# Optimization experiments

Hardware: AMD Instinct MI355X
Metric: run time of the kernel (lower is better)

Reference implementation:

```python
import jax, jax.numpy as jnp
import numpy as np

N_NODES = 50000
N_EDGES = 400000
N_GRAPHS = 64
DIMS = [3, 24, 48, 192]


def gcn_conv(x, src, dst, deg_inv_sqrt, W, b, num_nodes):
    # PyG GCNConv: x' = D^{-1/2} (A + I) D^{-1/2} (X W) + b
    h = x @ W  # [N, out]
    norm = deg_inv_sqrt[src] * deg_inv_sqrt[dst]  # [E2]
    msg = h[src] * norm[:, None]  # gather + scale, [E2, out]
    out = jax.ops.segment_sum(msg, dst, num_segments=num_nodes)
    return out + b


def setup_inputs() -> dict:
    key = jax.random.key(0)
    ks = jax.random.split(key, 10)
    node_features = jax.random.normal(ks[0], (N_NODES, DIMS[0]), dtype=jnp.float32)
    edge_indices = jax.random.randint(ks[1], (2, N_EDGES), 0, N_NODES, dtype=jnp.int64)
    batch_indices = jnp.sort(jax.random.randint(ks[2], (N_NODES,), 0, N_GRAPHS, dtype=jnp.int64))
    params = {}
    for i in range(3):
        fan_in, fan_out = DIMS[i], DIMS[i + 1]
        scale = 1.0 / np.sqrt(fan_in)
        params[f"W{i+1}"] = jax.random.uniform(ks[3 + 2 * i], (fan_in, fan_out), minval=-scale, maxval=scale, dtype=jnp.float32)
        params[f"b{i+1}"] = jnp.zeros((fan_out,), dtype=jnp.float32)
    return dict(node_features=node_features, edge_indices=edge_indices,
                batch_indices=batch_indices, **params)


def reference(node_features, edge_indices, batch_indices, W1, b1, W2, b2, W3, b3):
    num_nodes = node_features.shape[0]
    # add self-loops once, shared across the three convs
    loops = jnp.arange(num_nodes, dtype=edge_indices.dtype)
    src = jnp.concatenate([edge_indices[0], loops])
    dst = jnp.concatenate([edge_indices[1], loops])
    deg = jax.ops.segment_sum(jnp.ones_like(dst, dtype=node_features.dtype), dst,
                              num_segments=num_nodes)
    deg_inv_sqrt = jnp.where(deg > 0, jax.lax.rsqrt(jnp.maximum(deg, 1e-12)), 0.0)

    x = gcn_conv(node_features, src, dst, deg_inv_sqrt, W1, b1, num_nodes)
    x = gcn_conv(x, src, dst, deg_inv_sqrt, W2, b2, num_nodes)
    x = gcn_conv(x, src, dst, deg_inv_sqrt, W3, b3, num_nodes)

    # mean aggregation over nodes per graph
    sums = jax.ops.segment_sum(x, batch_indices, num_segments=N_GRAPHS)
    counts = jax.ops.segment_sum(jnp.ones((num_nodes,), dtype=x.dtype), batch_indices,
                                 num_segments=N_GRAPHS)
    return sums / jnp.maximum(counts, 1.0)[:, None]
```

## Files before the change

kernel.cpp:

```cpp
#include <hip/hip_runtime.h>

#define NN 50000
#define NE 400000
#define NG 64
#define NBK 196
#define CAP 2560
#define SB 98
#define EPB 4096

typedef unsigned int uint32;
typedef unsigned short uint16;


static __device__ __forceinline__ float wsum(float v) {
#pragma unroll
  for (int o = 32; o > 0; o >>= 1) v += __shfl_xor(v, o, 64);
  return v;
}

__global__ void __launch_bounds__(256) k_init(
    const float* __restrict__ x, const float* __restrict__ W1,
    const float* __restrict__ b1, const float* __restrict__ W2,
    const float* __restrict__ b2, const float* __restrict__ W3,
    float* __restrict__ W123, float* __restrict__ bW23, float* __restrict__ bW3,
    uint32* __restrict__ rsv, float* __restrict__ pooled, float* __restrict__ A) {
  int t = threadIdx.x, b = blockIdx.x;
  if (b == NBK) {
    __shared__ float w12[144];
    __shared__ float t48[48];
    if (t < 144) {
      int i = t / 48, k = t % 48;
      float s = 0.f;
      for (int j = 0; j < 24; ++j) s += W1[i * 24 + j] * W2[j * 48 + k];
      w12[t] = s;
    }
    if (t < 48) {
      float s = 0.f;
      for (int j = 0; j < 24; ++j) s += b1[j] * W2[j * 48 + t];
      t48[t] = s;
    }
    __syncthreads();
    if (t < 192) {
      float a0 = 0, a1 = 0, a2 = 0, ab = 0, ab3 = 0;
      for (int k = 0; k < 48; ++k) {
        float w3 = W3[k * 192 + t];
        a0 += w12[k] * w3;
        a1 += w12[48 + k] * w3;
        a2 += w12[96 + k] * w3;
        ab += t48[k] * w3;
        ab3 += b2[k] * w3;
      }
      W123[t] = a0;
      W123[192 + t] = a1;
      W123[384 + t] = a2;
      bW23[t] = ab;
      bW3[t] = ab3;
    }
    return;
  }
  if (b == 0) {
    rsv[t] = 0u;
    pooled[t] = 0.f;
    pooled[256 + t] = 0.f;
  }
  int n = b * 256 + t;
  if (n < NN) {
    float4 v;
    v.x = x[3 * n + 0];
    v.y = x[3 * n + 1];
    v.z = x[3 * n + 2];
    v.w = 1.0f;
    reinterpret_cast<float4*>(A)[n] = v;
  }
}

__global__ void __launch_bounds__(256) k_bscat(const int* __restrict__ src,
                                               const int* __restrict__ dst,
                                               uint32* __restrict__ rsv,
                                               uint32* __restrict__ ebuf) {
  __shared__ uint32 cnt[256];
  __shared__ uint32 base[256];
  int t = threadIdx.x;
  cnt[t] = 0u;
  __syncthreads();
  uint32 pk[16];
  uint32 bk[16];
  int e0 = blockIdx.x * EPB + t;
#pragma unroll
  for (int k = 0; k < 16; ++k) {
    int e = e0 + k * 256;
    uint32 b = 0xFFFFFFFFu, p = 0u;
    if (e < NE) {
      uint32 s = (uint32)src[e], d = (uint32)dst[e];
      b = d >> 8;
      p = s | ((d & 255u) << 16);
      atomicAdd(&cnt[b], 1u);
    }
    pk[k] = p;
    bk[k] = b;
  }
  __syncthreads();
  {
    uint32 c = cnt[t];
    base[t] = c ? (t * CAP + atomicAdd(&rsv[t], c)) : 0u;
    cnt[t] = 0u;
  }
  __syncthreads();
#pragma unroll
  for (int k = 0; k < 16; ++k) {
    if (bk[k] != 0xFFFFFFFFu) {
      uint32 slot = base[bk[k]] + atomicAdd(&cnt[bk[k]], 1u);
      ebuf[slot] = pk[k];
    }
  }
}

__global__ void __launch_bounds__(256) k_csr(const uint32* __restrict__ rsv,
                                             const uint32* __restrict__ ebuf,
                                             uint16* __restrict__ csr,
                                             uint2* __restrict__ offse,
                                             float2* __restrict__ drr,
                                             float* __restrict__ A) {
  __shared__ uint32 cnt[256];
  __shared__ uint32 scn[256];
  int b = blockIdx.x, t = threadIdx.x;
  uint32 lo = (uint32)b * CAP;
  uint32 hi = lo + rsv[b];
  cnt[t] = 0u;
  __syncthreads();
  for (uint32 i = lo + t; i < hi; i += 256) atomicAdd(&cnt[ebuf[i] >> 16], 1u);
  __syncthreads();
  uint32 c = cnt[t];
  scn[t] = c;
  __syncthreads();
  for (int o = 1; o < 256; o <<= 1) {
    uint32 u = (t >= o) ? scn[t - o] : 0u;
    __syncthreads();
    scn[t] += u;
    __syncthreads();
  }
  uint32 excl = scn[t] - c;
  cnt[t] = excl;
  int n = b * 256 + t;
  if (n < NN) {
    uint2 oe;
    oe.x = lo + excl;
    oe.y = lo + excl + c;
    offse[n] = oe;
    float deg = (float)(c + 1u);
    float ds = rsqrtf(deg);
    float2 dr;
    dr.x = 1.0f / deg;
    dr.y = sqrtf(deg);
    drr[n] = dr;
    float4 v4 = reinterpret_cast<const float4*>(A)[n];
    v4.x *= ds; v4.y *= ds; v4.z *= ds; v4.w *= ds;
    reinterpret_cast<float4*>(A)[n] = v4;
  }
  __syncthreads();
  for (uint32 i = lo + t; i < hi; i += 256) {
    uint32 p = ebuf[i];
    uint32 slot = atomicAdd(&cnt[p >> 16], 1u);
    csr[lo + slot] = (uint16)p;
  }
}

__global__ void k_gather(const uint2* __restrict__ offse,
                         const uint16* __restrict__ csr,
                         const float2* __restrict__ drr,
                         const float* __restrict__ zin, float* __restrict__ zout) {
  int tid = blockIdx.x * blockDim.x + threadIdx.x;
  int n = tid >> 2, ln = tid & 3;
  if (n >= NN) return;
  uint2 oe = offse[n];
  float4 acc = make_float4(0.f, 0.f, 0.f, 0.f);
  for (uint32 i = oe.x + ln; i < oe.y; i += 4) {
    uint32 s = csr[i];
    float4 v = reinterpret_cast<const float4*>(zin)[s];
    acc.x += v.x; acc.y += v.y; acc.z += v.z; acc.w += v.w;
  }
#pragma unroll
  for (int o = 1; o < 4; o <<= 1) {
    acc.x += __shfl_xor(acc.x, o, 64);
    acc.y += __shfl_xor(acc.y, o, 64);
    acc.z += __shfl_xor(acc.z, o, 64);
    acc.w += __shfl_xor(acc.w, o, 64);
  }
  if (ln == 0) {
    float4 zs = reinterpret_cast<const float4*>(zin)[n];
    float w = drr[n].x;
    float4 o4;
    o4.x = (acc.x + zs.x) * w;
    o4.y = (acc.y + zs.y) * w;
    o4.z = (acc.z + zs.z) * w;
    o4.w = (acc.w + zs.w) * w;
    reinterpret_cast<float4*>(zout)[n] = o4;
  }
}

__global__ void k_gather3_pool(const uint2* __restrict__ offse,
                               const uint16* __restrict__ csr,
                               const float2* __restrict__ drr,
                               const int* __restrict__ batch,
                               const float* __restrict__ B,
                               const float* __restrict__ C2,
                               float* __restrict__ pooled) {
  int tid = blockIdx.x * blockDim.x + threadIdx.x;
  int n = tid >> 2, ln = tid & 3;
  if (n >= NN) return;
  uint2 oe = offse[n];
  float ax = 0.f, ay = 0.f, az = 0.f;
  for (uint32 i = oe.x + ln; i < oe.y; i += 4) {
    uint32 s = csr[i];
    float4 v = reinterpret_cast<const float4*>(C2)[s];
    ax += v.x; ay += v.y; az += v.z;
  }
#pragma unroll
  for (int o = 1; o < 4; o <<= 1) {
    ax += __shfl_xor(ax, o, 64);
    ay += __shfl_xor(ay, o, 64);
    az += __shfl_xor(az, o, 64);
  }
  int g = batch[n];
  float vx = 0, vy = 0, vz = 0, v1 = 0, v2 = 0, cc = 0;
  if (ln == 0) {
    float4 zs = reinterpret_cast<const float4*>(C2)[n];
    float2 dr = drr[n];
    float rr = dr.y;
    float wr = dr.x * rr;
    vx = (ax + zs.x) * wr;
    vy = (ay + zs.y) * wr;
    vz = (az + zs.z) * wr;
    v1 = zs.w * rr;
    v2 = B[4 * n + 3] * rr;
    cc = 1.0f;
  }
  int g0 = __shfl(g, 0, 64);
  bool uni = __all(g == g0);
  if (uni) {
    float sx = wsum(vx), sy = wsum(vy), sz = wsum(vz);
    float s1 = wsum(v1), s2 = wsum(v2), sc = wsum(cc);
    if ((threadIdx.x & 63) == 0) {
      float* p = pooled + 8 * g0;
      atomicAdd(p + 0, sx); atomicAdd(p + 1, sy); atomicAdd(p + 2, sz);
      atomicAdd(p + 3, s1); atomicAdd(p + 4, s2); atomicAdd(p + 5, sc);
    }
  } else if (ln == 0) {
    float* p = pooled + 8 * g;
    atomicAdd(p + 0, vx); atomicAdd(p + 1, vy); atomicAdd(p + 2, vz);
    atomicAdd(p + 3, v1); atomicAdd(p + 4, v2); atomicAdd(p + 5, cc);
  }
}

__global__ void k_final(const float* __restrict__ pooled, const float* __restrict__ W123,
                        const float* __restrict__ bW23, const float* __restrict__ bW3,
                        const float* __restrict__ b3, float* __restrict__ out) {
  int g = blockIdx.x;
  int l = threadIdx.x;
  const float* p = pooled + 8 * g;
  float ic = 1.0f / fmaxf(p[5], 1.0f);
  float sx = p[0] * ic, sy = p[1] * ic, sz = p[2] * ic;
  float v1 = p[3] * ic, v2 = p[4] * ic;
  out[g * 192 + l] = sx * W123[l] + sy * W123[192 + l] + sz * W123[384 + l] +
                     v1 * bW23[l] + v2 * bW3[l] + b3[l];
}

extern "C" void kernel_launch(void* const* d_in, const int* in_sizes, int n_in,
                              void* d_out, int out_size, void* d_ws, size_t ws_size,
                              hipStream_t stream) {
  const float* x = (const float*)d_in[0];
  const int* edges = (const int*)d_in[1];
  const int* batch = (const int*)d_in[2];
  const float* W1 = (const float*)d_in[3];
  const float* b1 = (const float*)d_in[4];
  const float* W2 = (const float*)d_in[5];
  const float* b2 = (const float*)d_in[6];
  const float* W3 = (const float*)d_in[7];
  const float* b3 = (const float*)d_in[8];
  float* out = (float*)d_out;

  const int* src = edges;
  const int* dst = edges + NE;

  float* ws = (float*)d_ws;
  uint32* rsv = (uint32*)ws;
  uint2* offse = (uint2*)(ws + 256);
  float2* drr = (float2*)(ws + 100256);
  float* A = ws + 200256;
  float* B = ws + 400256;
  float* C2 = ws + 600256;
  uint32* ebuf = (uint32*)(ws + 800256);
  uint16* csr = (uint16*)(ws + 1302016);
  float* pooled = ws + 1552896;
  float* W123 = ws + 1553408;
  float* bW23 = ws + 1553984;
  float* bW3 = ws + 1554176;

  dim3 b256(256);
  dim3 bg((NN * 4 + 255) / 256);

  k_init<<<NBK + 1, b256, 0, stream>>>(x, W1, b1, W2, b2, W3, W123, bW23, bW3,
                                       rsv, pooled, A);
  k_bscat<<<SB, b256, 0, stream>>>(src, dst, rsv, ebuf);
  k_csr<<<NBK, b256, 0, stream>>>(rsv, ebuf, csr, offse, drr, A);

  k_gather<<<bg, b256, 0, stream>>>(offse, csr, drr, A, B);
  k_gather<<<bg, b256, 0, stream>>>(offse, csr, drr, B, C2);
  k_gather3_pool<<<bg, b256, 0, stream>>>(offse, csr, drr, batch, B, C2, pooled);

  k_final<<<NG, 192, 0, stream>>>(pooled, W123, bW23, bW3, b3, out);
}
```

Baseline: 61.33 us.

## Fuse edge bucketing into init kernel and final projection into last gather

Edge bucket-scatter now runs inside the init kernel. Each of 49 edge blocks writes into private per-(block,bucket) slots with fixed capacity, which removes the global reservation atomics. The CSR kernel reads these per-block segments using the stored counts. The final per-graph projection is folded into the last gather kernel through a last-block-done counter, so two launches are dropped. The risks are that the fixed CAPB of 96 can overflow on skewed inputs, and that the CSR build now strides over padded slots.

New measurement: 99.90 us. 1.63x slower.

```diff
diff --git a/kernel.cpp b/kernel.cpp
--- a/kernel.cpp
+++ b/kernel.cpp
@@ -5,8 +5,10 @@
 #define NG 64
 #define NBK 196
 #define CAP 2560
-#define SB 98
-#define EPB 4096
+#define SB 49
+#define EPB 8192
+#define CAPB 96
+#define NGB 782
 
 typedef unsigned int uint32;
 typedef unsigned short uint16;
@@ -18,13 +20,33 @@
   return v;
 }
 
-__global__ void __launch_bounds__(256) k_init(
-    const float* __restrict__ x, const float* __restrict__ W1,
+__global__ void __launch_bounds__(256) k_prep(
+    const float* __restrict__ x, const int* __restrict__ src,
+    const int* __restrict__ dst, const float* __restrict__ W1,
     const float* __restrict__ b1, const float* __restrict__ W2,
     const float* __restrict__ b2, const float* __restrict__ W3,
     float* __restrict__ W123, float* __restrict__ bW23, float* __restrict__ bW3,
-    uint32* __restrict__ rsv, float* __restrict__ pooled, float* __restrict__ A) {
+    uint32* __restrict__ cnts, uint32* __restrict__ ebuf,
+    float* __restrict__ pooled, uint32* __restrict__ done,
+    float* __restrict__ A) {
   int t = threadIdx.x, b = blockIdx.x;
+  if (b < NBK) {
+    if (b == 0) {
+      pooled[t] = 0.f;
+      pooled[256 + t] = 0.f;
+      if (t == 0) *done = 0u;
+    }
+    int n = b * 256 + t;
+    if (n < NN) {
+      float4 v;
+      v.x = x[3 * n + 0];
+      v.y = x[3 * n + 1];
+      v.z = x[3 * n + 2];
+      v.w = 1.0f;
+      reinterpret_cast<float4*>(A)[n] = v;
+    }
+    return;
+  }
   if (b == NBK) {
     __shared__ float w12[144];
     __shared__ float t48[48];
@@ -58,77 +80,48 @@
     }
     return;
   }
-  if (b == 0) {
-    rsv[t] = 0u;
-    pooled[t] = 0.f;
-    pooled[256 + t] = 0.f;
-  }
-  int n = b * 256 + t;
-  if (n < NN) {
-    float4 v;
-    v.x = x[3 * n + 0];
-    v.y = x[3 * n + 1];
-    v.z = x[3 * n + 2];
-    v.w = 1.0f;
-    reinterpret_cast<float4*>(A)[n] = v;
-  }
-}
-
-__global__ void __launch_bounds__(256) k_bscat(const int* __restrict__ src,
-                                               const int* __restrict__ dst,
-                                               uint32* __restrict__ rsv,
-                                               uint32* __restrict__ ebuf) {
-  __shared__ uint32 cnt[256];
-  __shared__ uint32 base[256];
-  int t = threadIdx.x;
-  cnt[t] = 0u;
-  __syncthreads();
-  uint32 pk[16];
-  uint32 bk[16];
-  int e0 = blockIdx.x * EPB + t;
-#pragma unroll
-  for (int k = 0; k < 16; ++k) {
-    int e = e0 + k * 256;
-    uint32 b = 0xFFFFFFFFu, p = 0u;
-    if (e < NE) {
-      uint32 s = (uint32)src[e], d = (uint32)dst[e];
-      b = d >> 8;
-      p = s | ((d & 255u) << 16);
-      atomicAdd(&cnt[b], 1u);
-    }
-    pk[k] = p;
-    bk[k] = b;
-  }
-  __syncthreads();
   {
+    __shared__ uint32 cnt[256];
+    int blk = b - (NBK + 1);
+    int e0 = blk * EPB;
+    int e1 = (e0 + EPB < NE) ? (e0 + EPB) : NE;
+    cnt[t] = 0u;
+    __syncthreads();
+    for (int e = e0 + t; e < e1; e += 256)
+      atomicAdd(&cnt[((uint32)dst[e]) >> 8], 1u);
+    __syncthreads();
     uint32 c = cnt[t];
-    base[t] = c ? (t * CAP + atomicAdd(&rsv[t], c)) : 0u;
+    if (t < NBK) cnts[blk * NBK + t] = c;
+    __syncthreads();
     cnt[t] = 0u;
-  }
-  __syncthreads();
-#pragma unroll
-  for (int k = 0; k < 16; ++k) {
-    if (bk[k] != 0xFFFFFFFFu) {
-      uint32 slot = base[bk[k]] + atomicAdd(&cnt[bk[k]], 1u);
-      ebuf[slot] = pk[k];
-    }
-  }
-}
-
-__global__ void __launch_bounds__(256) k_csr(const uint32* __restrict__ rsv,
+    __syncthreads();
+    for (int e = e0 + t; e < e1; e += 256) {
+      uint32 s = (uint32)src[e], d = (uint32)dst[e], bb = d >> 8;
+      uint32 slot = atomicAdd(&cnt[bb], 1u);
+      ebuf[(blk * NBK + bb) * CAPB + slot] = s | ((d & 255u) << 16);
+    }
+  }
+}
+
+__global__ void __launch_bounds__(256) k_csr(const uint32* __restrict__ cnts,
                                              const uint32* __restrict__ ebuf,
                                              uint16* __restrict__ csr,
                                              uint2* __restrict__ offse,
                                              float2* __restrict__ drr,
                                              float* __restrict__ A) {
+  __shared__ uint32 cntL[SB];
   __shared__ uint32 cnt[256];
   __shared__ uint32 scn[256];
   int b = blockIdx.x, t = threadIdx.x;
-  uint32 lo = (uint32)b * CAP;
-  uint32 hi = lo + rsv[b];
+  if (t < SB) cntL[t] = cnts[t * NBK + b];
   cnt[t] = 0u;
   __syncthreads();
-  for (uint32 i = lo + t; i < hi; i += 256) atomicAdd(&cnt[ebuf[i] >> 16], 1u);
+  const int TOT = SB * CAPB;
+  for (int i = t; i < TOT; i += 256) {
+    int blk = i / CAPB, idx = i - blk * CAPB;
+    if ((uint32)idx < cntL[blk])
+      atomicAdd(&cnt[ebuf[(blk * NBK + b) * CAPB + idx] >> 16], 1u);
+  }
   __syncthreads();
   uint32 c = cnt[t];
   scn[t] = c;
@@ -141,6 +134,7 @@
   }
   uint32 excl = scn[t] - c;
   cnt[t] = excl;
+  uint32 lo = (uint32)b * CAP;
   int n = b * 256 + t;
   if (n < NN) {
     uint2 oe;
@@ -158,10 +152,13 @@
     reinterpret_cast<float4*>(A)[n] = v4;
   }
   __syncthreads();
-  for (uint32 i = lo + t; i < hi; i += 256) {
-    uint32 p = ebuf[i];
-    uint32 slot = atomicAdd(&cnt[p >> 16], 1u);
-    csr[lo + slot] = (uint16)p;
+  for (int i = t; i < TOT; i += 256) {
+    int blk = i / CAPB, idx = i - blk * CAPB;
+    if ((uint32)idx < cntL[blk]) {
+      uint32 p = ebuf[(blk * NBK + b) * CAPB + idx];
+      uint32 slot = atomicAdd(&cnt[p >> 16], 1u);
+      csr[lo + slot] = (uint16)p;
+    }
   }
 }
 
@@ -198,71 +195,85 @@
   }
 }
 
-__global__ void k_gather3_pool(const uint2* __restrict__ offse,
-                               const uint16* __restrict__ csr,
-                               const float2* __restrict__ drr,
-                               const int* __restrict__ batch,
-                               const float* __restrict__ B,
-                               const float* __restrict__ C2,
-                               float* __restrict__ pooled) {
+__global__ void __launch_bounds__(256) k_g3pf(
+    const uint2* __restrict__ offse, const uint16* __restrict__ csr,
+    const float2* __restrict__ drr, const int* __restrict__ batch,
+    const float* __restrict__ B,
+    const float* __restrict__ C2,
+    float* __restrict__ pooled, uint32* __restrict__ done,
+    const float* __restrict__ W123, const float* __restrict__ bW23,
+    const float* __restrict__ bW3, const float* __restrict__ b3,
+    float* __restrict__ out) {
   int tid = blockIdx.x * blockDim.x + threadIdx.x;
   int n = tid >> 2, ln = tid & 3;
-  if (n >= NN) return;
-  uint2 oe = offse[n];
-  float ax = 0.f, ay = 0.f, az = 0.f;
-  for (uint32 i = oe.x + ln; i < oe.y; i += 4) {
-    uint32 s = csr[i];
-    float4 v = reinterpret_cast<const float4*>(C2)[s];
-    ax += v.x; ay += v.y; az += v.z;
-  }
+  if (n < NN) {
+    uint2 oe = offse[n];
+    float ax = 0.f, ay = 0.f, az = 0.f;
+    for (uint32 i = oe.x + ln; i < oe.y; i += 4) {
+      uint32 s = csr[i];
+      float4 v = reinterpret_cast<const float4*>(C2)[s];
+      ax += v.x; ay += v.y; az += v.z;
+    }
 #pragma unroll
-  for (int o = 1; o < 4; o <<= 1) {
-    ax += __shfl_xor(ax, o, 64);
-    ay += __shfl_xor(ay, o, 64);
-    az += __shfl_xor(az, o, 64);
-  }
-  int g = batch[n];
-  float vx = 0, vy = 0, vz = 0, v1 = 0, v2 = 0, cc = 0;
-  if (ln == 0) {
-    float4 zs = reinterpret_cast<const float4*>(C2)[n];
-    float2 dr = drr[n];
-    float rr = dr.y;
-    float wr = dr.x * rr;
-    vx = (ax + zs.x) * wr;
-    vy = (ay + zs.y) * wr;
-    vz = (az + zs.z) * wr;
-    v1 = zs.w * rr;
-    v2 = B[4 * n + 3] * rr;
-    cc = 1.0f;
-  }
-  int g0 = __shfl(g, 0, 64);
-  bool uni = __all(g == g0);
-  if (uni) {
-    float sx = wsum(vx), sy = wsum(vy), sz = wsum(vz);
-    float s1 = wsum(v1), s2 = wsum(v2), sc = wsum(cc);
-    if ((threadIdx.x & 63) == 0) {
-      float* p = pooled + 8 * g0;
-      atomicAdd(p + 0, sx); atomicAdd(p + 1, sy); atomicAdd(p + 2, sz);
-      atomicAdd(p + 3, s1); atomicAdd(p + 4, s2); atomicAdd(p + 5, sc);
-    }
-  } else if (ln == 0) {
-    float* p = pooled + 8 * g;
-    atomicAdd(p + 0, vx); atomicAdd(p + 1, vy); atomicAdd(p + 2, vz);
-    atomicAdd(p + 3, v1); atomicAdd(p + 4, v2); atomicAdd(p + 5, cc);
-  }
-}
-
-__global__ void k_final(const float* __restrict__ pooled, const float* __restrict__ W123,
-                        const float* __restrict__ bW23, const float* __restrict__ bW3,
-                        const float* __restrict__ b3, float* __restrict__ out) {
-  int g = blockIdx.x;
-  int l = threadIdx.x;
-  const float* p = pooled + 8 * g;
-  float ic = 1.0f / fmaxf(p[5], 1.0f);
-  float sx = p[0] * ic, sy = p[1] * ic, sz = p[2] * ic;
-  float v1 = p[3] * ic, v2 = p[4] * ic;
-  out[g * 192 + l] = sx * W123[l] + sy * W123[192 + l] + sz * W123[384 + l] +
-                     v1 * bW23[l] + v2 * bW3[l] + b3[l];
+    for (int o = 1; o < 4; o <<= 1) {
+      ax += __shfl_xor(ax, o, 64);
+      ay += __shfl_xor(ay, o, 64);
+      az += __shfl_xor(az, o, 64);
+    }
+    int g = batch[n];
+    float vx = 0, vy = 0, vz = 0, v1 = 0, v2 = 0, cc = 0;
+    if (ln == 0) {
+      float4 zs = reinterpret_cast<const float4*>(C2)[n];
+      float2 dr = drr[n];
+      float rr = dr.y;
+      float wr = dr.x * rr;
+      vx = (ax + zs.x) * wr;
+      vy = (ay + zs.y) * wr;
+      vz = (az + zs.z) * wr;
+      v1 = zs.w * rr;
+      v2 = B[4 * n + 3] * rr;
+      cc = 1.0f;
+    }
+    int g0 = __shfl(g, 0, 64);
+    bool uni = __all(g == g0);
+    if (uni) {
+      float sx = wsum(vx), sy = wsum(vy), sz = wsum(vz);
+      float s1 = wsum(v1), s2 = wsum(v2), sc = wsum(cc);
+      if ((threadIdx.x & 63) == 0) {
+        float* p = pooled + 8 * g0;
+        atomicAdd(p + 0, sx); atomicAdd(p + 1, sy); atomicAdd(p + 2, sz);
+        atomicAdd(p + 3, s1); atomicAdd(p + 4, s2); atomicAdd(p + 5, sc);
+      }
+    } else if (ln == 0) {
+      float* p = pooled + 8 * g;
+      atomicAdd(p + 0, vx); atomicAdd(p + 1, vy); atomicAdd(p + 2, vz);
+      atomicAdd(p + 3, v1); atomicAdd(p + 4, v2); atomicAdd(p + 5, cc);
+    }
+  }
+  __shared__ int lastf;
+  __syncthreads();
+  if (threadIdx.x == 0) {
+    __threadfence();
+    uint32 d = __hip_atomic_fetch_add(done, 1u, __ATOMIC_ACQ_REL,
+                                      __HIP_MEMORY_SCOPE_AGENT);
+    lastf = (d == (uint32)(gridDim.x - 1)) ? 1 : 0;
+  }
+  __syncthreads();
+  if (lastf) {
+    for (int i = threadIdx.x; i < NG * 192; i += 256) {
+      int g = i / 192, l = i - g * 192;
+      const float* p = pooled + 8 * g;
+      float cn = __hip_atomic_load(p + 5, __ATOMIC_RELAXED, __HIP_MEMORY_SCOPE_AGENT);
+      float ic = 1.0f / fmaxf(cn, 1.0f);
+      float sx = __hip_atomic_load(p + 0, __ATOMIC_RELAXED, __HIP_MEMORY_SCOPE_AGENT) * ic;
+      float sy = __hip_atomic_load(p + 1, __ATOMIC_RELAXED, __HIP_MEMORY_SCOPE_AGENT) * ic;
+      float sz = __hip_atomic_load(p + 2, __ATOMIC_RELAXED, __HIP_MEMORY_SCOPE_AGENT) * ic;
+      float v1 = __hip_atomic_load(p + 3, __ATOMIC_RELAXED, __HIP_MEMORY_SCOPE_AGENT) * ic;
+      float v2 = __hip_atomic_load(p + 4, __ATOMIC_RELAXED, __HIP_MEMORY_SCOPE_AGENT) * ic;
+      out[i] = sx * W123[l] + sy * W123[192 + l] + sz * W123[384 + l] +
+               v1 * bW23[l] + v2 * bW3[l] + b3[l];
+    }
+  }
 }
 
 extern "C" void kernel_launch(void* const* d_in, const int* in_sizes, int n_in,
@@ -283,30 +294,29 @@
   const int* dst = edges + NE;
 
   float* ws = (float*)d_ws;
-  uint32* rsv = (uint32*)ws;
-  uint2* offse = (uint2*)(ws + 256);
-  float2* drr = (float2*)(ws + 100256);
-  float* A = ws + 200256;
-  float* B = ws + 400256;
-  float* C2 = ws + 600256;
-  uint32* ebuf = (uint32*)(ws + 800256);
-  uint16* csr = (uint16*)(ws + 1302016);
-  float* pooled = ws + 1552896;
-  float* W123 = ws + 1553408;
-  float* bW23 = ws + 1553984;
-  float* bW3 = ws + 1554176;
+  uint32* cnts = (uint32*)ws;
+  uint2* offse = (uint2*)(ws + 9728);
+  float2* drr = (float2*)(ws + 109728);
+  float* A = ws + 209728;
+  float* B = ws + 409728;
+  float* C2 = ws + 609728;
+  uint32* ebuf = (uint32*)(ws + 809728);
+  uint16* csr = (uint16*)(ws + 1731712);
+  float* pooled = ws + 1982592;
+  float* W123 = ws + 1983104;
+  float* bW23 = ws + 1983680;
+  float* bW3 = ws + 1983872;
+  uint32* done = (uint32*)(ws + 1984064);
 
   dim3 b256(256);
-  dim3 bg((NN * 4 + 255) / 256);
-
-  k_init<<<NBK + 1, b256, 0, stream>>>(x, W1, b1, W2, b2, W3, W123, bW23, bW3,
-                                       rsv, pooled, A);
-  k_bscat<<<SB, b256, 0, stream>>>(src, dst, rsv, ebuf);
-  k_csr<<<NBK, b256, 0, stream>>>(rsv, ebuf, csr, offse, drr, A);
-
-  k_gather<<<bg, b256, 0, stream>>>(offse, csr, drr, A, B);
-  k_gather<<<bg, b256, 0, stream>>>(offse, csr, drr, B, C2);
-  k_gather3_pool<<<bg, b256, 0, stream>>>(offse, csr, drr, batch, B, C2, pooled);
-
-  k_final<<<NG, 192, 0, stream>>>(pooled, W123, bW23, bW3, b3, out);
-}
+
+  k_prep<<<NBK + 1 + SB, b256, 0, stream>>>(x, src, dst, W1, b1, W2, b2, W3,
+                                            W123, bW23, bW3, cnts, ebuf,
+                                            pooled, done, A);
+  k_csr<<<NBK, b256, 0, stream>>>(cnts, ebuf, csr, offse, drr, A);
+
+  k_gather<<<NGB, b256, 0, stream>>>(offse, csr, drr, A, B);
+  k_gather<<<NGB, b256, 0, stream>>>(offse, csr, drr, B, C2);
+  k_g3pf<<<NGB, b256, 0, stream>>>(offse, csr, drr, batch, B, C2, pooled, done,
+                                   W123, bW23, bW3, b3, out);
+}
```
